# Kernel tuning notes

Measured on AMD Instinct MI355X. Metric: run time of the kernel, lower is better.

## Reference

```python
import jax, jax.numpy as jnp
import numpy as np

B, CIN, COUT, H, W, K, G = 2, 256, 256, 128, 128, 3, 4
PAD = (K - 1) // 2


def setup_inputs() -> dict:
    key = jax.random.key(0)
    k1, k2, k3, k4 = jax.random.split(key, 4)
    x = jax.random.normal(k1, (B, CIN, H, W), dtype=jnp.float32)
    # conv_offset: 1x1 conv, out channels = G*2*K*K. (Zero-init in the module; use
    # small random weights so offsets are non-trivial for correctness testing.)
    w_offset = jax.random.normal(k2, (G * 2 * K * K, CIN), dtype=jnp.float32) * 0.01
    b_offset = jax.random.normal(k3, (G * 2 * K * K,), dtype=jnp.float32) * 0.5
    # DeformConv weight (bias=False in mmcv DeformConv)
    w_deform = jax.random.normal(k4, (COUT, CIN, K, K), dtype=jnp.float32) * (1.0 / np.sqrt(CIN * K * K))
    return {"x": x, "w_offset": w_offset, "b_offset": b_offset, "w_deform": w_deform}


def _bilinear_gather(img, y, x):
    """img: [B,G,Cg,H,W]; y,x: [B,G,H,W] float sample coords -> [B,G,Cg,H,W].
    Zero padding outside the image (mmcv DCN bilinear semantics)."""
    b, g, cg, h, w = img.shape
    imgf = img.reshape(b, g, cg, h * w)
    y0 = jnp.floor(y)
    x0 = jnp.floor(x)
    out = jnp.zeros((b, g, cg, h * w), img.dtype)
    for yy, xx in ((y0, x0), (y0, x0 + 1.0), (y0 + 1.0, x0), (y0 + 1.0, x0 + 1.0)):
        wgt = (1.0 - jnp.abs(y - yy)) * (1.0 - jnp.abs(x - xx))
        valid = (yy >= 0) & (yy < h) & (xx >= 0) & (xx < w)
        wgt = jnp.where(valid, wgt, 0.0)
        yi = jnp.clip(yy, 0, h - 1).astype(jnp.int32)
        xi = jnp.clip(xx, 0, w - 1).astype(jnp.int32)
        idx = (yi * w + xi).reshape(b, g, 1, h * w)
        vals = jnp.take_along_axis(imgf, jnp.broadcast_to(idx, (b, g, cg, h * w)), axis=3)
        out = out + wgt.reshape(b, g, 1, h * w) * vals
    return out.reshape(b, g, cg, h, w)


def reference(x, w_offset, b_offset, w_deform):
    b, cin, h, w = x.shape
    cout, _, k, _ = w_deform.shape
    pad = (k - 1) // 2
    # 1x1 offset conv
    offset = jnp.einsum('bchw,oc->bohw', x, w_offset) + b_offset[None, :, None, None]
    g = offset.shape[1] // (2 * k * k)
    off = offset.reshape(b, g, k * k, 2, h, w)  # (dy, dx) per kernel tap, mmcv layout
    xg = x.reshape(b, g, cin // g, h, w)
    hh = jnp.arange(h, dtype=x.dtype)[:, None]
    ww = jnp.arange(w, dtype=x.dtype)[None, :]
    out = jnp.zeros((b, cout, h, w), x.dtype)
    for i in range(k):
        for j in range(k):
            t = i * k + j
            ys = hh - pad + i + off[:, :, t, 0]  # [B,G,H,W]
            xs = ww - pad + j + off[:, :, t, 1]
            samp = _bilinear_gather(xg, ys, xs).reshape(b, cin, h, w)
            out = out + jnp.einsum('bchw,oc->bohw', samp, w_deform[:, :, i, j])
    return jax.nn.relu(out)
```

## Files before the change

kernel.cpp:

```cpp
#include <hip/hip_runtime.h>
#include <stdint.h>

#define HW    16384
#define CIN   256
#define COUT  256
#define Hh    128
#define Ww    128
#define OFFC  72

typedef __attribute__((ext_vector_type(4))) float    f32x4;
typedef __attribute__((ext_vector_type(2))) _Float16 f16x2;
typedef __attribute__((ext_vector_type(8))) _Float16 f16x8;
typedef unsigned short u16;
typedef unsigned int   u32;

__device__ __forceinline__ u16 f2h(float f) { return __builtin_bit_cast(u16, (_Float16)f); }
__device__ __forceinline__ u32 pk2(float f) { u32 h = f2h(f); return h | (h << 16); }
__device__ __forceinline__ f16x2 bch(u32 u) { return __builtin_bit_cast(f16x2, u); }

__global__ __launch_bounds__(256) void kprep(const float* __restrict__ x, const float* __restrict__ wd,
                                             const float* __restrict__ wo, u16* __restrict__ xt,
                                             u16* __restrict__ wfrag, u16* __restrict__ wfrag2) {
  __shared__ float smem[64 * 129];
  int blk = blockIdx.x;
  if (blk < 1024) {
    int bg = blk >> 7;
    int p0 = (blk & 127) << 7;
    const float* src = x + (size_t)bg * 64 * HW + p0;
    #pragma unroll
    for (int r = 0; r < 8; ++r) {
      int idx = (threadIdx.x + 256 * r) * 4;
      int c = idx >> 7, px = idx & 127;
      f32x4 v = *(const f32x4*)(src + (size_t)c * HW + px);
      smem[c * 129 + px + 0] = v[0];
      smem[c * 129 + px + 1] = v[1];
      smem[c * 129 + px + 2] = v[2];
      smem[c * 129 + px + 3] = v[3];
    }
    __syncthreads();
    int px = threadIdx.x >> 1, seg = threadIdx.x & 1;
    u32 w[16];
    #pragma unroll
    for (int k = 0; k < 16; ++k) {
      float lo = smem[(seg * 32 + 2 * k) * 129 + px];
      float hi = smem[(seg * 32 + 2 * k + 1) * 129 + px];
      w[k] = (u32)f2h(lo) | ((u32)f2h(hi) << 16);
    }
    u16* dst = xt + ((size_t)bg * HW + p0 + px) * 64 + seg * 32;
    *(uint4*)(dst + 0)  = make_uint4(w[0],  w[1],  w[2],  w[3]);
    *(uint4*)(dst + 8)  = make_uint4(w[4],  w[5],  w[6],  w[7]);
    *(uint4*)(dst + 16) = make_uint4(w[8],  w[9],  w[10], w[11]);
    *(uint4*)(dst + 24) = make_uint4(w[12], w[13], w[14], w[15]);
  } else if (blk < 1152) {
    int bb = blk - 1024;
    int nh = bb & 31;
    int g  = bb >> 5;
    const float* src = wd + (size_t)(nh * 8) * 2304 + (size_t)g * 64 * 9;
    #pragma unroll
    for (int r = 0; r < 18; ++r) {
      int idx = threadIdx.x + 256 * r;
      int cl  = idx / 576;
      int rem = idx - cl * 576;
      smem[cl * 576 + rem] = src[(size_t)cl * 2304 + rem];
    }
    __syncthreads();
    int nt = nh >> 1, nb = (nh & 1) * 8;
    #pragma unroll
    for (int r = 0; r < 18; ++r) {
      int o  = threadIdx.x + 256 * r;
      int j  = o & 7;
      int n8 = (o >> 3) & 7;
      int q  = (o >> 6) & 3;
      int kcl = o >> 8;
      int t = kcl >> 1, half = kcl & 1;
      int cg = half * 32 + q * 8 + j;
      float v = smem[n8 * 576 + cg * 9 + t];
      int kc = (g * 9 + t) * 2 + half;
      int lane = q * 16 + nb + n8;
      wfrag[((size_t)(kc * 16 + nt) * 64 + lane) * 8 + j] = f2h(v);
    }
  } else {
    int e = (blk - 1152) * 256 + threadIdx.x;
    int j = e & 7;
    int lane = (e >> 3) & 63;
    int idx = e >> 9;
    int kc = idx / 5, nt = idx - 5 * kc;
    int n16 = lane & 15, q = lane >> 4;
    int oc = nt * 16 + n16;
    int c  = kc * 32 + q * 8 + j;
    float v = (oc < OFFC) ? wo[(size_t)oc * CIN + c] : 0.f;
    wfrag2[e] = f2h(v);
  }
}

__device__ __forceinline__ void mkpre(float yy, float xx, int* ob, u32* wp) {
  float y0f = floorf(yy), x0f = floorf(xx);
  float fy = yy - y0f, fx = xx - x0f;
  int y0 = (int)y0f, x0 = (int)x0f;
  int y1 = y0 + 1, x1 = x0 + 1;
  float vy0 = (y0 >= 0 && y0 < Hh) ? 1.f : 0.f;
  float vy1 = (y1 >= 0 && y1 < Hh) ? 1.f : 0.f;
  float vx0 = (x0 >= 0 && x0 < Ww) ? 1.f : 0.f;
  float vx1 = (x1 >= 0 && x1 < Ww) ? 1.f : 0.f;
  wp[0] = pk2((1.f - fy) * (1.f - fx) * vy0 * vx0);
  wp[1] = pk2((1.f - fy) * fx * vy0 * vx1);
  wp[2] = pk2(fy * (1.f - fx) * vy1 * vx0);
  wp[3] = pk2(fy * fx * vy1 * vx1);
  int cy0 = min(max(y0, 0), Hh - 1), cy1 = min(max(y1, 0), Hh - 1);
  int cx0 = min(max(x0, 0), Ww - 1), cx1 = min(max(x1, 0), Ww - 1);
  ob[0] = (cy0 * Ww + cx0) << 7;
  ob[1] = (cy0 * Ww + cx1) << 7;
  ob[2] = (cy1 * Ww + cx0) << 7;
  ob[3] = (cy1 * Ww + cx1) << 7;
}

__device__ __forceinline__ uint4 bil16(const uint4* v, const u32* wp) {
  f16x2 W0 = bch(wp[0]), W1 = bch(wp[1]), W2 = bch(wp[2]), W3 = bch(wp[3]);
  uint4 r;
  { f16x2 s = bch(v[0].x) * W0 + bch(v[1].x) * W1 + bch(v[2].x) * W2 + bch(v[3].x) * W3; r.x = __builtin_bit_cast(u32, s); }
  { f16x2 s = bch(v[0].y) * W0 + bch(v[1].y) * W1 + bch(v[2].y) * W2 + bch(v[3].y) * W3; r.y = __builtin_bit_cast(u32, s); }
  { f16x2 s = bch(v[0].z) * W0 + bch(v[1].z) * W1 + bch(v[2].z) * W2 + bch(v[3].z) * W3; r.z = __builtin_bit_cast(u32, s); }
  { f16x2 s = bch(v[0].w) * W0 + bch(v[1].w) * W1 + bch(v[2].w) * W2 + bch(v[3].w) * W3; r.w = __builtin_bit_cast(u32, s); }
  return r;
}

__global__ __launch_bounds__(512) void k2(const u16* __restrict__ xt, const u16* __restrict__ wfrag2,
                                          const float* __restrict__ bo, const u16* __restrict__ wfrag,
                                          float* __restrict__ out) {
  __shared__ u16   astage[2 * 8 * 512];
  __shared__ float offl[64 * 74];
  int tid  = threadIdx.x;
  int lane = tid & 63, n16 = lane & 15, q = (tid >> 4) & 3;
  int wv   = tid >> 6;
  int sp   = wv >> 1;
  int hp   = wv & 1;
  int b  = blockIdx.x >> 8;
  int p0 = (blockIdx.x & 255) << 6;
  int h  = p0 >> 7, w0 = p0 & 127;
  const char* xtb = (const char*)xt + (size_t)b * 4 * HW * 128;
  float fh  = (float)h;
  float fxp = (float)(w0 + sp * 16 + n16);
  int   chb = hp * 64 + q * 16;

  f32x4 acc[4][2];
  #pragma unroll
  for (int mt = 0; mt < 4; ++mt) {
    acc[mt][0] = (f32x4){0.f, 0.f, 0.f, 0.f};
    acc[mt][1] = (f32x4){0.f, 0.f, 0.f, 0.f};
  }

  if (wv < 4) {
    f32x4 oacc[5];
    #pragma unroll
    for (int nt = 0; nt < 5; ++nt) {
      int oc = nt * 16 + n16;
      float bv = (oc < OFFC) ? bo[oc] : 0.f;
      oacc[nt] = (f32x4){bv, bv, bv, bv};
    }
    #pragma unroll
    for (int kc = 0; kc < 8; ++kc) {
      int g = kc >> 1;
      f16x8 af = __builtin_bit_cast(f16x8, *(const uint4*)(xtb +
          ((size_t)(g * HW + p0 + wv * 16 + n16)) * 128 + (kc & 1) * 64 + q * 16));
      #pragma unroll
      for (int nt = 0; nt < 5; ++nt) {
        f16x8 bfo = __builtin_bit_cast(f16x8, *(const uint4*)(wfrag2 + (size_t)(((kc * 5 + nt) << 6) + lane) * 8));
        oacc[nt] = __builtin_amdgcn_mfma_f32_16x16x32_f16(af, bfo, oacc[nt], 0, 0, 0);
      }
    }
    #pragma unroll
    for (int nt = 0; nt < 5; ++nt) {
      int oc = nt * 16 + n16;
      if (oc < OFFC) {
        #pragma unroll
        for (int r = 0; r < 4; ++r)
          offl[(wv * 16 + q * 4 + r) * 74 + oc] = oacc[nt][r];
      }
    }
  }
  uint4 bf0[2];
  bf0[0] = *(const uint4*)(wfrag + ((size_t)(wv * 2 + 0) * 64 + lane) * 8);
  bf0[1] = *(const uint4*)(wfrag + ((size_t)(wv * 2 + 1) * 64 + lane) * 8);
  __syncthreads();

  uint4 dA[4], dB[4];
  u32   wpA[4], wpB[4];

  auto issue = [&](int gt, uint4* dd, u32* wpp) {
    int pxl = sp * 16 + n16;
    float oy = offl[pxl * 74 + gt * 2];
    float ox = offl[pxl * 74 + gt * 2 + 1];
    int g = (gt * 57) >> 9;
    int t = gt - g * 9;
    int i = (t * 683) >> 11;
    int j = t - i * 3;
    int ob[4];
    mkpre(fh + (float)(i - 1) + oy, fxp + (float)(j - 1) + ox, ob, wpp);
    const char* xg = xtb + (size_t)g * HW * 128;
    #pragma unroll
    for (int c = 0; c < 4; ++c)
      dd[c] = *(const uint4*)(xg + ob[c] + chb);
  };
  auto consume = [&](int slot, int gt) {
    uint4 bf1[2];
    const u16* wb1 = wfrag + ((size_t)((2 * gt + 1) * 16 + wv * 2) * 64 + lane) * 8;
    bf1[0] = *(const uint4*)(wb1);
    bf1[1] = *(const uint4*)(wb1 + 512);
    #pragma unroll
    for (int mt = 0; mt < 4; ++mt) {
      f16x8 af = __builtin_bit_cast(f16x8,
          *(const uint4*)&astage[(slot * 8 + mt * 2 + 0) * 512 + lane * 8]);
      acc[mt][0] = __builtin_amdgcn_mfma_f32_16x16x32_f16(af, __builtin_bit_cast(f16x8, bf0[0]), acc[mt][0], 0, 0, 0);
      acc[mt][1] = __builtin_amdgcn_mfma_f32_16x16x32_f16(af, __builtin_bit_cast(f16x8, bf0[1]), acc[mt][1], 0, 0, 0);
    }
    #pragma unroll
    for (int mt = 0; mt < 4; ++mt) {
      f16x8 af = __builtin_bit_cast(f16x8,
          *(const uint4*)&astage[(slot * 8 + mt * 2 + 1) * 512 + lane * 8]);
      acc[mt][0] = __builtin_amdgcn_mfma_f32_16x16x32_f16(af, __builtin_bit_cast(f16x8, bf1[0]), acc[mt][0], 0, 0, 0);
      acc[mt][1] = __builtin_amdgcn_mfma_f32_16x16x32_f16(af, __builtin_bit_cast(f16x8, bf1[1]), acc[mt][1], 0, 0, 0);
    }
    if (gt < 35) {
      const u16* wb0 = wfrag + ((size_t)((2 * gt + 2) * 16 + wv * 2) * 64 + lane) * 8;
      bf0[0] = *(const uint4*)(wb0);
      bf0[1] = *(const uint4*)(wb0 + 512);
    }
  };

  issue(0, dA, wpA);
  issue(1, dB, wpB);
  *(uint4*)&astage[(0 * 8 + sp * 2 + hp) * 512 + lane * 8] = bil16(dA, wpA);
  __syncthreads();

  #pragma unroll 1
  for (int gt = 0; gt < 36; gt += 2) {
    *(uint4*)&astage[(1 * 8 + sp * 2 + hp) * 512 + lane * 8] = bil16(dB, wpB);
    if (gt + 2 < 36) issue(gt + 2, dA, wpA);
    consume(0, gt);
    __syncthreads();
    if (gt + 2 < 36) {
      *(uint4*)&astage[(0 * 8 + sp * 2 + hp) * 512 + lane * 8] = bil16(dA, wpA);
      issue(gt + 3, dB, wpB);
    }
    consume(1, gt + 1);
    __syncthreads();
  }

  float* op = out + (size_t)b * COUT * HW + p0;
  #pragma unroll
  for (int mt = 0; mt < 4; ++mt)
    #pragma unroll
    for (int j = 0; j < 2; ++j) {
      f32x4 v = acc[mt][j];
      #pragma unroll
      for (int r = 0; r < 4; ++r) v[r] = fmaxf(v[r], 0.f);
      int cout = wv * 32 + j * 16 + n16;
      *(f32x4*)(op + (size_t)cout * HW + mt * 16 + q * 4) = v;
    }
}

extern "C" void kernel_launch(void* const* d_in, const int* in_sizes, int n_in,
                              void* d_out, int out_size, void* d_ws, size_t ws_size,
                              hipStream_t stream) {
  const float* x  = (const float*)d_in[0];
  const float* wo = (const float*)d_in[1];
  const float* bo = (const float*)d_in[2];
  const float* wd = (const float*)d_in[3];
  float* out = (float*)d_out;

  u16* xtp    = (u16*)d_ws;
  u16* wfrag  = (u16*)((char*)d_ws + 16777216);
  u16* wfrag2 = (u16*)((char*)d_ws + 16777216 + 1179648);

  kprep<<<1232, 256, 0, stream>>>(x, wd, wo, xtp, wfrag, wfrag2);
  k2   <<<512,  512, 0, stream>>>(xtp, wfrag2, bo, wfrag, out);
}
```

Before: 180.6 us.

## Use barriers that skip vmcnt drain, raise MFMA priority, coalesce prep stores

Replaces __syncthreads in the main deformable-conv loop with a barrier that waits only on LDS counters (lgkmcnt), so the in-flight global gathers issued for the next tap are not drained at each barrier. The MFMA block is wrapped in s_setprio so the math wave is favored while other waves issue loads. The transpose in the prep kernel is reorganized so consecutive threads write consecutive 16-byte chunks, giving coalesced stores. The custom barrier relies on the compiler inserting the correct vmcnt waits before the gathered data is used.

```diff
diff --git a/kernel.cpp b/kernel.cpp
--- a/kernel.cpp
+++ b/kernel.cpp
@@ -17,6 +17,13 @@
 __device__ __forceinline__ u16 f2h(float f) { return __builtin_bit_cast(u16, (_Float16)f); }
 __device__ __forceinline__ u32 pk2(float f) { u32 h = f2h(f); return h | (h << 16); }
 __device__ __forceinline__ f16x2 bch(u32 u) { return __builtin_bit_cast(f16x2, u); }
+
+__device__ __forceinline__ void bar_nodrain() {
+  asm volatile("s_waitcnt lgkmcnt(0)" ::: "memory");
+  __builtin_amdgcn_sched_barrier(0);
+  __builtin_amdgcn_s_barrier();
+  __builtin_amdgcn_sched_barrier(0);
+}
 
 __global__ __launch_bounds__(256) void kprep(const float* __restrict__ x, const float* __restrict__ wd,
                                              const float* __restrict__ wo, u16* __restrict__ xt,
@@ -38,19 +45,20 @@
       smem[c * 129 + px + 3] = v[3];
     }
     __syncthreads();
-    int px = threadIdx.x >> 1, seg = threadIdx.x & 1;
-    u32 w[16];
-    #pragma unroll
-    for (int k = 0; k < 16; ++k) {
-      float lo = smem[(seg * 32 + 2 * k) * 129 + px];
-      float hi = smem[(seg * 32 + 2 * k + 1) * 129 + px];
-      w[k] = (u32)f2h(lo) | ((u32)f2h(hi) << 16);
-    }
-    u16* dst = xt + ((size_t)bg * HW + p0 + px) * 64 + seg * 32;
-    *(uint4*)(dst + 0)  = make_uint4(w[0],  w[1],  w[2],  w[3]);
-    *(uint4*)(dst + 8)  = make_uint4(w[4],  w[5],  w[6],  w[7]);
-    *(uint4*)(dst + 16) = make_uint4(w[8],  w[9],  w[10], w[11]);
-    *(uint4*)(dst + 24) = make_uint4(w[12], w[13], w[14], w[15]);
+    u16* dstb = xt + ((size_t)bg * HW + p0) * 64;
+    #pragma unroll
+    for (int k = 0; k < 4; ++k) {
+      int e  = k * 256 + threadIdx.x;
+      int px = e >> 3, ck = e & 7;
+      u32 w[4];
+      #pragma unroll
+      for (int m = 0; m < 4; ++m) {
+        float lo = smem[(ck * 8 + 2 * m + 0) * 129 + px];
+        float hi = smem[(ck * 8 + 2 * m + 1) * 129 + px];
+        w[m] = (u32)f2h(lo) | ((u32)f2h(hi) << 16);
+      }
+      *(uint4*)(dstb + (size_t)e * 8) = make_uint4(w[0], w[1], w[2], w[3]);
+    }
   } else if (blk < 1152) {
     int bb = blk - 1024;
     int nh = bb & 31;
@@ -206,6 +214,7 @@
     const u16* wb1 = wfrag + ((size_t)((2 * gt + 1) * 16 + wv * 2) * 64 + lane) * 8;
     bf1[0] = *(const uint4*)(wb1);
     bf1[1] = *(const uint4*)(wb1 + 512);
+    __builtin_amdgcn_s_setprio(1);
     #pragma unroll
     for (int mt = 0; mt < 4; ++mt) {
       f16x8 af = __builtin_bit_cast(f16x8,
@@ -220,6 +229,7 @@
       acc[mt][0] = __builtin_amdgcn_mfma_f32_16x16x32_f16(af, __builtin_bit_cast(f16x8, bf1[0]), acc[mt][0], 0, 0, 0);
       acc[mt][1] = __builtin_amdgcn_mfma_f32_16x16x32_f16(af, __builtin_bit_cast(f16x8, bf1[1]), acc[mt][1], 0, 0, 0);
     }
+    __builtin_amdgcn_s_setprio(0);
     if (gt < 35) {
       const u16* wb0 = wfrag + ((size_t)((2 * gt + 2) * 16 + wv * 2) * 64 + lane) * 8;
       bf0[0] = *(const uint4*)(wb0);
@@ -230,20 +240,20 @@
   issue(0, dA, wpA);
   issue(1, dB, wpB);
   *(uint4*)&astage[(0 * 8 + sp * 2 + hp) * 512 + lane * 8] = bil16(dA, wpA);
-  __syncthreads();
+  bar_nodrain();
 
   #pragma unroll 1
   for (int gt = 0; gt < 36; gt += 2) {
     *(uint4*)&astage[(1 * 8 + sp * 2 + hp) * 512 + lane * 8] = bil16(dB, wpB);
     if (gt + 2 < 36) issue(gt + 2, dA, wpA);
     consume(0, gt);
-    __syncthreads();
+    bar_nodrain();
     if (gt + 2 < 36) {
       *(uint4*)&astage[(0 * 8 + sp * 2 + hp) * 512 + lane * 8] = bil16(dA, wpA);
       issue(gt + 3, dB, wpB);
     }
     consume(1, gt + 1);
-    __syncthreads();
+    bar_nodrain();
   }
 
   float* op = out + (size_t)b * COUT * HW + p0;
```

Result: slower. 198.2 us (+9.7%).

## Rework input transpose with smaller tiles, packed fp16 LDS and block swizzle

Applied to the files above, without the earlier changes.

The x-to-fp16 channel-last transpose now uses 64-pixel tiles across twice as many blocks. Channel pairs are converted and packed into u32 before the LDS write, and a rotated index avoids bank conflicts, which shrinks the shared footprint and raises occupancy of the prep kernel. The main kernel also remaps block indices with an XCD-style swizzle so neighbouring pixel tiles land on the same die for better L2 reuse. The risks are more blocks in the prep kernel and a different cache locality pattern in the main kernel.

```diff
diff --git a/kernel.cpp b/kernel.cpp
--- a/kernel.cpp
+++ b/kernel.cpp
@@ -21,38 +21,41 @@
 __global__ __launch_bounds__(256) void kprep(const float* __restrict__ x, const float* __restrict__ wd,
                                              const float* __restrict__ wo, u16* __restrict__ xt,
                                              u16* __restrict__ wfrag, u16* __restrict__ wfrag2) {
-  __shared__ float smem[64 * 129];
+  __shared__ float smem[8 * 576];
   int blk = blockIdx.x;
-  if (blk < 1024) {
-    int bg = blk >> 7;
-    int p0 = (blk & 127) << 7;
-    const float* src = x + (size_t)bg * 64 * HW + p0;
-    #pragma unroll
-    for (int r = 0; r < 8; ++r) {
-      int idx = (threadIdx.x + 256 * r) * 4;
-      int c = idx >> 7, px = idx & 127;
-      f32x4 v = *(const f32x4*)(src + (size_t)c * HW + px);
-      smem[c * 129 + px + 0] = v[0];
-      smem[c * 129 + px + 1] = v[1];
-      smem[c * 129 + px + 2] = v[2];
-      smem[c * 129 + px + 3] = v[3];
-    }
-    __syncthreads();
-    int px = threadIdx.x >> 1, seg = threadIdx.x & 1;
-    u32 w[16];
-    #pragma unroll
-    for (int k = 0; k < 16; ++k) {
-      float lo = smem[(seg * 32 + 2 * k) * 129 + px];
-      float hi = smem[(seg * 32 + 2 * k + 1) * 129 + px];
-      w[k] = (u32)f2h(lo) | ((u32)f2h(hi) << 16);
-    }
-    u16* dst = xt + ((size_t)bg * HW + p0 + px) * 64 + seg * 32;
-    *(uint4*)(dst + 0)  = make_uint4(w[0],  w[1],  w[2],  w[3]);
-    *(uint4*)(dst + 8)  = make_uint4(w[4],  w[5],  w[6],  w[7]);
-    *(uint4*)(dst + 16) = make_uint4(w[8],  w[9],  w[10], w[11]);
-    *(uint4*)(dst + 24) = make_uint4(w[12], w[13], w[14], w[15]);
-  } else if (blk < 1152) {
-    int bb = blk - 1024;
+  if (blk < 2048) {
+    int bg = blk >> 8;
+    int p0 = (blk & 255) << 6;
+    int pq = threadIdx.x & 15;
+    int cs = threadIdx.x >> 4;
+    const float* src = x + (size_t)bg * 64 * HW + p0 + pq * 4;
+    u32* lds = (u32*)smem;
+    #pragma unroll
+    for (int s = 0; s < 2; ++s) {
+      int c2 = cs + 16 * s;
+      f32x4 lo = *(const f32x4*)(src + (size_t)(2 * c2 + 0) * HW);
+      f32x4 hi = *(const f32x4*)(src + (size_t)(2 * c2 + 1) * HW);
+      #pragma unroll
+      for (int j = 0; j < 4; ++j) {
+        int px = pq * 4 + j;
+        u32 pkv = (u32)f2h(lo[j]) | ((u32)f2h(hi[j]) << 16);
+        lds[px * 36 + ((c2 + px) & 31)] = pkv;
+      }
+    }
+    __syncthreads();
+    u16* dstb = xt + ((size_t)bg * HW + p0) * 64;
+    #pragma unroll
+    for (int r = 0; r < 2; ++r) {
+      int e  = r * 256 + threadIdx.x;
+      int px = e >> 3, c4 = e & 7;
+      u32 w[4];
+      #pragma unroll
+      for (int m = 0; m < 4; ++m)
+        w[m] = lds[px * 36 + ((4 * c4 + m + px) & 31)];
+      *(uint4*)(dstb + (size_t)e * 8) = make_uint4(w[0], w[1], w[2], w[3]);
+    }
+  } else if (blk < 2176) {
+    int bb = blk - 2048;
     int nh = bb & 31;
     int g  = bb >> 5;
     const float* src = wd + (size_t)(nh * 8) * 2304 + (size_t)g * 64 * 9;
@@ -80,7 +83,7 @@
       wfrag[((size_t)(kc * 16 + nt) * 64 + lane) * 8 + j] = f2h(v);
     }
   } else {
-    int e = (blk - 1152) * 256 + threadIdx.x;
+    int e = (blk - 2176) * 256 + threadIdx.x;
     int j = e & 7;
     int lane = (e >> 3) & 63;
     int idx = e >> 9;
@@ -134,8 +137,10 @@
   int wv   = tid >> 6;
   int sp   = wv >> 1;
   int hp   = wv & 1;
-  int b  = blockIdx.x >> 8;
-  int p0 = (blockIdx.x & 255) << 6;
+  int blk  = blockIdx.x;
+  int swz  = (blk & 7) * 64 + (blk >> 3);
+  int b  = swz >> 8;
+  int p0 = (swz & 255) << 6;
   int h  = p0 >> 7, w0 = p0 & 127;
   const char* xtb = (const char*)xt + (size_t)b * 4 * HW * 128;
   float fh  = (float)h;
@@ -272,6 +277,6 @@
   u16* wfrag  = (u16*)((char*)d_ws + 16777216);
   u16* wfrag2 = (u16*)((char*)d_ws + 16777216 + 1179648);
 
-  kprep<<<1232, 256, 0, stream>>>(x, wd, wo, xtp, wfrag, wfrag2);
+  kprep<<<2256, 256, 0, stream>>>(x, wd, wo, xtp, wfrag, wfrag2);
   k2   <<<512,  512, 0, stream>>>(xtp, wfrag2, bo, wfrag, out);
 }
```

After: 178.2 us. Within noise of the previous version (-1.3%).
